# Kernel optimization log

Measured on AMD Instinct MI355X. Metric: run time of the kernel, lower is better.

## Reference

```python
import jax, jax.numpy as jnp
import numpy as np


def _hard_sigmoid(x):
    # torch: clamp(0.2 * x + 0.5, 0, 1)
    return jnp.clip(0.2 * x + 0.5, 0.0, 1.0)


def _hardtanh(x):
    return jnp.clip(x, -1.0, 1.0)


def _run_dir(x, h0, c0, w_ih, w_hh, b):
    """One direction of a HardLSTM layer.
    x: [T, B, I], h0/c0: [B, H], w_ih: [4H, I], w_hh: [4H, H], b: [4H]
    (b is bias_ih + bias_hh of the original cell; identical math).
    """
    # Hoist the input projection out of the recurrence (one big GEMM).
    gx = jnp.einsum('tbi,gi->tbg', x, w_ih) + b  # [T, B, 4H]

    def step(carry, gx_t):
        h, c = carry
        gates = gx_t + h @ w_hh.T  # [B, 4H]
        i, f, g, o = jnp.split(gates, 4, axis=-1)
        i = _hard_sigmoid(i)
        f = _hard_sigmoid(f)
        g = _hardtanh(g)
        o = _hard_sigmoid(o)
        cy = f * c + i * g
        hy = o * _hardtanh(cy)
        return (hy, cy), hy

    (h, c), ys = jax.lax.scan(step, (h0, c0), gx)
    return ys, h, c


def _bidir_layer(x, h0, c0, w_ih, w_hh, b):
    """h0/c0: [2, B, H]; w_ih: [2, 4H, I]; w_hh: [2, 4H, H]; b: [2, 4H]."""
    yf, hf, cf = _run_dir(x, h0[0], c0[0], w_ih[0], w_hh[0], b[0])
    yb, hb, cb = _run_dir(x[::-1], h0[1], c0[1], w_ih[1], w_hh[1], b[1])
    yb = yb[::-1]
    # torch cat([yf.unsqueeze(2), yb.unsqueeze(2)], 2).view(T, B, 2H)
    y = jnp.concatenate([yf, yb], axis=-1)  # [T, B, 2H]
    return y, jnp.stack([hf, hb]), jnp.stack([cf, cb])


def reference(x, h0, c0, w_ih0, w_hh0, b0, w_ih1, w_hh1, b1):
    # Stacked 2-layer bidirectional HardLSTM, time-major input.
    y0, h_l0, c_l0 = _bidir_layer(x, h0[0:2], c0[0:2], w_ih0, w_hh0, b0)
    y1, h_l1, c_l1 = _bidir_layer(y0, h0[2:4], c0[2:4], w_ih1, w_hh1, b1)
    hn = jnp.concatenate([h_l0, h_l1], axis=0)  # [4, B, H]
    cn = jnp.concatenate([c_l0, c_l1], axis=0)
    return y1, hn, cn


def setup_inputs() -> dict:
    key = jax.random.key(0)
    ks = jax.random.split(key, 8)
    T, B, I, H = 512, 32, 512, 1024
    stdv = 1.0 / np.sqrt(H)  # matches reset_parameters uniform(-stdv, stdv) scale
    FGB = 1.0  # forget_gate_bias

    x = jax.random.normal(ks[0], (T, B, I), dtype=jnp.float32)
    h0 = jnp.zeros((4, B, H), dtype=jnp.float32)
    c0 = jnp.zeros((4, B, H), dtype=jnp.float32)

    def mk_w(k, shape):
        return (jax.random.normal(k, shape, dtype=jnp.float32) * stdv).astype(jnp.float32)

    w_ih0 = mk_w(ks[1], (2, 4 * H, I))
    w_hh0 = mk_w(ks[2], (2, 4 * H, H))
    b0 = mk_w(ks[3], (2, 4 * H))
    w_ih1 = mk_w(ks[4], (2, 4 * H, 2 * H))
    w_hh1 = mk_w(ks[5], (2, 4 * H, H))
    b1 = mk_w(ks[6], (2, 4 * H))
    # forget gate bias override (bias_ih forget slice = FGB, bias_hh = 0 -> sum = FGB)
    b0 = b0.at[:, H:2 * H].set(FGB)
    b1 = b1.at[:, H:2 * H].set(FGB)

    return {"x": x, "h0": h0, "c0": c0,
            "w_ih0": w_ih0, "w_hh0": w_hh0, "b0": b0,
            "w_ih1": w_ih1, "w_hh1": w_hh1, "b1": b1}
```

## Files before the change

kernel.cpp:

```cpp
#include <hip/hip_runtime.h>
#include <cstdint>


typedef _Float16 half8 __attribute__((ext_vector_type(8)));
typedef _Float16 half4v __attribute__((ext_vector_type(4)));
typedef float floatx4 __attribute__((ext_vector_type(4)));
typedef int int4v __attribute__((ext_vector_type(4)));

#define T_LEN 512
#define BATCH 32
#define HID 1024
#define NTB 16384
#define UPW 16
#define WPD 64

__device__ __forceinline__ float hsig(float x) {
  return fminf(fmaxf(fmaf(0.2f, x, 0.5f), 0.0f), 1.0f);
}
__device__ __forceinline__ float htanh(float x) {
  return fminf(fmaxf(x, -1.0f), 1.0f);
}

__device__ __forceinline__ int4v load_co16(const void* p) {
  int4v r;
  asm volatile("global_load_dwordx4 %0, %1, off sc0 sc1"
               : "=&v"(r) : "v"(p) : "memory");
  return r;
}
__device__ __forceinline__ void store_co16(void* p, int4v v) {
  asm volatile("global_store_dwordx4 %0, %1, off sc0 sc1"
               :: "v"(p), "v"(v) : "memory");
}
__device__ __forceinline__ void waitcnt0() {
  asm volatile("s_waitcnt vmcnt(0)" ::: "memory");
}
__device__ __forceinline__ void barrier_lgkm() {
  asm volatile("s_waitcnt lgkmcnt(0)" ::: "memory");
  __builtin_amdgcn_sched_barrier(0);
  __builtin_amdgcn_s_barrier();
  __builtin_amdgcn_sched_barrier(0);
}

__device__ __forceinline__ void gll16(const void* g, void* l) {
  __builtin_amdgcn_global_load_lds((const __attribute__((address_space(1))) void*)g,
                                   (__attribute__((address_space(3))) void*)l,
                                   16, 0, 0);
}

__device__ __forceinline__ void gate_xpose(floatx4 v, bool i1, bool i0,
                                           float& gI, float& gF,
                                           float& gG, float& gO) {
  float s0 = i1 ? v[0] : v[2], s1 = i1 ? v[1] : v[3];
  float r0 = __shfl_xor(s0, 32), r1 = __shfl_xor(s1, 32);
  float A0 = i1 ? r0 : v[0], A1 = i1 ? r1 : v[1];
  float A2 = i1 ? v[2] : r0, A3 = i1 ? v[3] : r1;
  s0 = i0 ? A0 : A1; s1 = i0 ? A2 : A3;
  r0 = __shfl_xor(s0, 16); r1 = __shfl_xor(s1, 16);
  gI = i0 ? r0 : A0; gF = i0 ? A1 : r0;
  gG = i0 ? r1 : A2; gO = i0 ? A3 : r1;
}

__global__ __launch_bounds__(256) void cvt_f32_f16(const float* __restrict__ s,
                                                   _Float16* __restrict__ d,
                                                   int n4) {
  int i = blockIdx.x * blockDim.x + threadIdx.x;
  int stride = gridDim.x * blockDim.x;
  for (; i < n4; i += stride) {
    float4 v = ((const float4*)s)[i];
    half4v h = {(_Float16)v.x, (_Float16)v.y, (_Float16)v.z, (_Float16)v.w};
    ((half4v*)d)[i] = h;
  }
}

__global__ __launch_bounds__(256) void gemm_gx(const _Float16* __restrict__ A,
                                               const _Float16* __restrict__ B,
                                               const float* __restrict__ bias,
                                               _Float16* __restrict__ C,
                                               int K) {
  __shared__ __align__(16) _Float16 A_s[128 * 64];
  __shared__ __align__(16) _Float16 B_s[128 * 64];
  const int tid = threadIdx.x;
  const int lane = tid & 63;
  const int w = tid >> 6;
  const int bm = blockIdx.x >> 7;
  const int bn = blockIdx.x & 127;
  const int m0 = bm * 128, n0 = bn * 128;

  floatx4 acc[4][4] = {};

  const int srow = w * 8 + (lane >> 3);
  const int scol = ((lane & 7) ^ ((lane >> 3) & 7)) * 8;
  const _Float16* Ag = A + (size_t)(m0 + srow) * K + scol;
  const _Float16* Bg = B + (size_t)(n0 + srow) * K + scol;
  char* As_base = (char*)A_s + (size_t)(w * 8) * 128;
  char* Bs_base = (char*)B_s + (size_t)(w * 8) * 128;

  const int wm = (w >> 1) * 64;
  const int wn = (w & 1) * 64;
  const int fr = lane & 15;
  const int fk = lane >> 4;

  for (int kb = 0; kb < K; kb += 64) {
#pragma unroll
    for (int i = 0; i < 4; ++i) {
      gll16(Ag + (size_t)i * 32 * K + kb, As_base + i * 32 * 128);
      gll16(Bg + (size_t)i * 32 * K + kb, Bs_base + i * 32 * 128);
    }
    __syncthreads();
#pragma unroll
    for (int kt = 0; kt < 2; ++kt) {
      half8 af[4], bf[4];
#pragma unroll
      for (int mi = 0; mi < 4; ++mi) {
        int row = wm + mi * 16 + fr;
        int k8 = kt * 4 + fk;
        af[mi] = *(const half8*)(A_s + row * 64 + ((k8 ^ (row & 7)) << 3));
      }
#pragma unroll
      for (int ni = 0; ni < 4; ++ni) {
        int row = wn + ni * 16 + fr;
        int k8 = kt * 4 + fk;
        bf[ni] = *(const half8*)(B_s + row * 64 + ((k8 ^ (row & 7)) << 3));
      }
#pragma unroll
      for (int mi = 0; mi < 4; ++mi)
#pragma unroll
        for (int ni = 0; ni < 4; ++ni)
          acc[mi][ni] = __builtin_amdgcn_mfma_f32_16x16x32_f16(af[mi], bf[ni],
                                                               acc[mi][ni], 0, 0, 0);
    }
    __syncthreads();
  }

#pragma unroll
  for (int mi = 0; mi < 4; ++mi) {
    int rowb = m0 + wm + mi * 16 + fk * 4;
#pragma unroll
    for (int r = 0; r < 4; ++r) {
      float bv = bias[rowb + r];
#pragma unroll
      for (int ni = 0; ni < 4; ++ni) {
        int col = n0 + wn + ni * 16 + fr;
        C[(size_t)(rowb + r) * NTB + col] = (_Float16)(acc[mi][ni][r] + bv);
      }
    }
  }
}

__global__ __launch_bounds__(512) void recur(const _Float16* __restrict__ gx,
                                             const _Float16* __restrict__ whh,
                                             const float* __restrict__ h0,
                                             const float* __restrict__ c0,
                                             _Float16* __restrict__ hbuf,
                                             int* __restrict__ flags,
                                             int layer,
                                             _Float16* __restrict__ yf16,
                                             float* __restrict__ yf32,
                                             float* __restrict__ hn,
                                             float* __restrict__ cn) {
  __shared__ __align__(16) _Float16 h_s[BATCH * HID];
  __shared__ __align__(16) _Float16 hout_s[BATCH * UPW];

  const int tid = threadIdx.x;
  const int lane = tid & 63;
  const int w = tid >> 6;
  const int wu = w >> 1, wn = w & 1;
  const int dir = blockIdx.x >> 6;
  const int wgd = blockIdx.x & 63;
  const int u0 = wgd * UPW;
  const int fr = lane & 15, fk = lane >> 4;

  half8 af[32];
  {
    const int g = fr >> 2, du = fr & 3;
    const _Float16* wrow = whh + ((size_t)dir * 4096 + g * 1024 + u0 + wu * 4 + du) * HID;
#pragma unroll
    for (int kt = 0; kt < 32; ++kt)
      af[kt] = *(const half8*)(wrow + kt * 32 + fk * 8);
  }

  const int unit = u0 + wu * 4 + fk;
  const int bat  = wn * 16 + fr;
  const size_t st0 = (size_t)(layer * 2 + dir) * (BATCH * HID);
  float c = c0[st0 + (size_t)bat * HID + unit];

  _Float16* buf0 = hbuf + (size_t)dir * (BATCH * HID);
  _Float16* buf1 = hbuf + (size_t)(2 + dir) * (BATCH * HID);
  int* fl = flags + dir * WPD;

  hout_s[bat * UPW + wu * 4 + fk] = (_Float16)h0[st0 + (size_t)bat * HID + unit];
  __syncthreads();
  if (w == 0) {
    int b = lane >> 1, hf = lane & 1;
    int4v v = *(const int4v*)(hout_s + b * UPW + hf * 8);
    store_co16(buf0 + (size_t)b * HID + u0 + hf * 8, v);
    waitcnt0();
    if (lane == 0) {
      int fv = 1;
      asm volatile("global_store_dword %0, %1, off sc0 sc1"
                   :: "v"(fl + wgd), "v"(fv) : "memory");
    }
  }

  const size_t GS = (size_t)1024 * NTB;
  const _Float16* gxp = gx + ((size_t)dir * 4096 + unit) * NTB;

  int ts0 = dir ? (T_LEN - 1) : 0;
  float gxi = (float)gxp[0 * GS + (size_t)ts0 * BATCH + bat];
  float gxf = (float)gxp[1 * GS + (size_t)ts0 * BATCH + bat];
  float gxg = (float)gxp[2 * GS + (size_t)ts0 * BATCH + bat];
  float gxo = (float)gxp[3 * GS + (size_t)ts0 * BATCH + bat];

  const bool i1 = (fk >> 1) & 1, i0 = fk & 1;

  for (int t = 0; t < T_LEN; ++t) {
    if (w == 0) {
      const int want = t + 1;
      for (;;) {
        int v;
        asm volatile("global_load_dword %0, %1, off sc0 sc1\n\ts_waitcnt vmcnt(0)"
                     : "=&v"(v) : "v"(fl + lane) : "memory");
        if (__all(v >= want)) break;
        __builtin_amdgcn_s_sleep(1);
      }
    }
    barrier_lgkm();

    const _Float16* src = (t & 1) ? buf1 : buf0;
    _Float16* dst = (t & 1) ? buf0 : buf1;

    int4v hv[8];
#pragma unroll
    for (int i = 0; i < 8; ++i)
      hv[i] = load_co16((const char*)src + (size_t)(i * 512 + tid) * 16);
    waitcnt0();
#pragma unroll
    for (int i = 0; i < 8; ++i) {
      int cbyte = (i * 512 + tid) * 16;
      int b = cbyte >> 11;
      int slot = cbyte & 2047;
      *(int4v*)((char*)h_s + b * 2048 + (slot ^ ((b & 7) << 4))) = hv[i];
    }

    int tn = (t + 1 < T_LEN) ? t + 1 : t;
    int tsn = dir ? (T_LEN - 1 - tn) : tn;
    float ngxi = (float)gxp[0 * GS + (size_t)tsn * BATCH + bat];
    float ngxf = (float)gxp[1 * GS + (size_t)tsn * BATCH + bat];
    float ngxg = (float)gxp[2 * GS + (size_t)tsn * BATCH + bat];
    float ngxo = (float)gxp[3 * GS + (size_t)tsn * BATCH + bat];

    barrier_lgkm();

    floatx4 acc0 = {0.f, 0.f, 0.f, 0.f}, acc1 = {0.f, 0.f, 0.f, 0.f};
    {
      const char* hp = (const char*)h_s + bat * 2048;
      const int bx = (bat & 7) << 4;
#pragma unroll
      for (int kt = 0; kt < 32; kt += 2) {
        half8 b0 = *(const half8*)(hp + ((kt * 64 + fk * 16) ^ bx));
        half8 b1 = *(const half8*)(hp + (((kt + 1) * 64 + fk * 16) ^ bx));
        acc0 = __builtin_amdgcn_mfma_f32_16x16x32_f16(af[kt], b0, acc0, 0, 0, 0);
        acc1 = __builtin_amdgcn_mfma_f32_16x16x32_f16(af[kt + 1], b1, acc1, 0, 0, 0);
      }
    }
    floatx4 v = acc0 + acc1;

    float gI, gF, gG, gO;
    gate_xpose(v, i1, i0, gI, gF, gG, gO);

    float ig = hsig(gI + gxi);
    float fg = hsig(gF + gxf);
    float gg = htanh(gG + gxg);
    float og = hsig(gO + gxo);
    c = fg * c + ig * gg;
    float h = og * htanh(c);

    hout_s[bat * UPW + wu * 4 + fk] = (_Float16)h;

    const int tseq = dir ? (T_LEN - 1 - t) : t;
    size_t yidx = ((size_t)tseq * BATCH + bat) * 2048 + (size_t)dir * 1024 + unit;
    if (yf16) yf16[yidx] = (_Float16)h;
    else      yf32[yidx] = h;

    gxi = ngxi; gxf = ngxf; gxg = ngxg; gxo = ngxo;

    if (t == T_LEN - 1) {
      size_t o = st0 + (size_t)bat * HID + unit;
      hn[o] = h;
      cn[o] = c;
    } else {
      barrier_lgkm();
      if (w == 0) {
        int b = lane >> 1, hf = lane & 1;
        int4v vv = *(const int4v*)(hout_s + b * UPW + hf * 8);
        store_co16(dst + (size_t)b * HID + u0 + hf * 8, vv);
        waitcnt0();
        if (lane == 0) {
          int fv = t + 2;
          asm volatile("global_store_dword %0, %1, off sc0 sc1"
                       :: "v"(fl + wgd), "v"(fv) : "memory");
        }
      }
    }
  }
}

extern "C" void kernel_launch(void* const* d_in, const int* in_sizes, int n_in,
                              void* d_out, int out_size, void* d_ws, size_t ws_size,
                              hipStream_t stream) {
  const float* x    = (const float*)d_in[0];
  const float* h0   = (const float*)d_in[1];
  const float* c0   = (const float*)d_in[2];
  const float* wih0 = (const float*)d_in[3];
  const float* whh0 = (const float*)d_in[4];
  const float* b0   = (const float*)d_in[5];
  const float* wih1 = (const float*)d_in[6];
  const float* whh1 = (const float*)d_in[7];
  const float* b1   = (const float*)d_in[8];
  float* out = (float*)d_out;

  char* ws = (char*)d_ws;
  size_t off = 0;
  int* flags = (int*)ws;                      off += 4096;
  _Float16* xh    = (_Float16*)(ws + off);    off += (size_t)8388608 * 2;
  _Float16* wih0h = (_Float16*)(ws + off);    off += (size_t)4194304 * 2;
  _Float16* whh0h = (_Float16*)(ws + off);    off += (size_t)8388608 * 2;
  _Float16* wih1h = (_Float16*)(ws + off);    off += (size_t)16777216 * 2;
  _Float16* whh1h = (_Float16*)(ws + off);    off += (size_t)8388608 * 2;
  _Float16* y0h   = (_Float16*)(ws + off);    off += (size_t)33554432 * 2;
  _Float16* hbuf  = (_Float16*)(ws + off);    off += (size_t)131072 * 2;
  _Float16* gxbuf = (_Float16*)(ws + off);    off += (size_t)134217728 * 2;

  hipMemsetAsync(flags, 0, 4096, stream);

  cvt_f32_f16<<<2048, 256, 0, stream>>>(x,    xh,    8388608 / 4);
  cvt_f32_f16<<<2048, 256, 0, stream>>>(wih0, wih0h, 4194304 / 4);
  cvt_f32_f16<<<2048, 256, 0, stream>>>(whh0, whh0h, 8388608 / 4);
  cvt_f32_f16<<<2048, 256, 0, stream>>>(wih1, wih1h, 16777216 / 4);
  cvt_f32_f16<<<2048, 256, 0, stream>>>(whh1, whh1h, 8388608 / 4);

  float* hn = out + 33554432;
  float* cn = out + 33685504;

  gemm_gx<<<8192, 256, 0, stream>>>(wih0h, xh, b0, gxbuf, 512);
  recur<<<128, 512, 0, stream>>>(gxbuf, whh0h, h0, c0, hbuf, flags, 0,
                                 y0h, nullptr, hn, cn);
  gemm_gx<<<8192, 256, 0, stream>>>(wih1h, y0h, b1, gxbuf, 2048);
  recur<<<128, 512, 0, stream>>>(gxbuf, whh1h, h0, c0, hbuf, flags + 128, 1,
                                 nullptr, out, hn, cn);
}
```

Before: 6.393 ms.

## Replace flag-based grid sync with tagged self-validating h chunks

Drops the separate flag array and the wave-0 spin-then-load handshake. Each wave now publishes its h values in 16-byte chunks that carry the step tag in the first and last dwords, so consumers poll the data itself and scatter it into LDS once both tags match. This removes a round trip (flag poll, then data load) and the LDS staging and barrier on the producer side. In exchange, every thread spin-loads its 256 bytes repeatedly, which adds polling traffic, and correctness depends on each 16-byte store being seen atomically.

```diff
diff --git a/kernel.cpp b/kernel.cpp
--- a/kernel.cpp
+++ b/kernel.cpp
@@ -6,6 +6,7 @@
 typedef _Float16 half4v __attribute__((ext_vector_type(4)));
 typedef float floatx4 __attribute__((ext_vector_type(4)));
 typedef int int4v __attribute__((ext_vector_type(4)));
+typedef int int2v __attribute__((ext_vector_type(2)));
 
 #define T_LEN 512
 #define BATCH 32
@@ -13,6 +14,7 @@
 #define NTB 16384
 #define UPW 16
 #define WPD 64
+#define CHUNKS_DIR 8192
 
 __device__ __forceinline__ float hsig(float x) {
   return fminf(fmaxf(fmaf(0.2f, x, 0.5f), 0.0f), 1.0f);
@@ -58,6 +60,20 @@
   r0 = __shfl_xor(s0, 16); r1 = __shfl_xor(s1, 16);
   gI = i0 ? r0 : A0; gF = i0 ? A1 : r0;
   gG = i0 ? r1 : A2; gO = i0 ? A3 : r1;
+}
+
+__device__ __forceinline__ void publish_h(float h, int tag, char* cb,
+                                          int wgd, int w, int fr, int fk) {
+  union { _Float16 f; unsigned short u; } cv; cv.f = (_Float16)h;
+  int hb = (int)cv.u;
+  int p = __shfl_xor(hb, 16);
+  int d01 = (fk & 1) ? ((p & 0xffff) | (hb << 16))
+                     : ((hb & 0xffff) | (p << 16));
+  int d23 = __shfl_xor(d01, 32);
+  if (fk == 0) {
+    int4v v = {tag, d01, d23, tag};
+    store_co16(cb + (size_t)(wgd * 128 + w * 16 + fr) * 16, v);
+  }
 }
 
 __global__ __launch_bounds__(256) void cvt_f32_f16(const float* __restrict__ s,
@@ -151,15 +167,13 @@
                                              const _Float16* __restrict__ whh,
                                              const float* __restrict__ h0,
                                              const float* __restrict__ c0,
-                                             _Float16* __restrict__ hbuf,
-                                             int* __restrict__ flags,
+                                             char* __restrict__ chunkbuf,
                                              int layer,
                                              _Float16* __restrict__ yf16,
                                              float* __restrict__ yf32,
                                              float* __restrict__ hn,
                                              float* __restrict__ cn) {
   __shared__ __align__(16) _Float16 h_s[BATCH * HID];
-  __shared__ __align__(16) _Float16 hout_s[BATCH * UPW];
 
   const int tid = threadIdx.x;
   const int lane = tid & 63;
@@ -170,6 +184,9 @@
   const int u0 = wgd * UPW;
   const int fr = lane & 15, fk = lane >> 4;
 
+  char* cb0 = chunkbuf + (size_t)(dir * 2 + 0) * CHUNKS_DIR * 16;
+  char* cb1 = chunkbuf + (size_t)(dir * 2 + 1) * CHUNKS_DIR * 16;
+
   half8 af[32];
   {
     const int g = fr >> 2, du = fr & 3;
@@ -184,23 +201,7 @@
   const size_t st0 = (size_t)(layer * 2 + dir) * (BATCH * HID);
   float c = c0[st0 + (size_t)bat * HID + unit];
 
-  _Float16* buf0 = hbuf + (size_t)dir * (BATCH * HID);
-  _Float16* buf1 = hbuf + (size_t)(2 + dir) * (BATCH * HID);
-  int* fl = flags + dir * WPD;
-
-  hout_s[bat * UPW + wu * 4 + fk] = (_Float16)h0[st0 + (size_t)bat * HID + unit];
-  __syncthreads();
-  if (w == 0) {
-    int b = lane >> 1, hf = lane & 1;
-    int4v v = *(const int4v*)(hout_s + b * UPW + hf * 8);
-    store_co16(buf0 + (size_t)b * HID + u0 + hf * 8, v);
-    waitcnt0();
-    if (lane == 0) {
-      int fv = 1;
-      asm volatile("global_store_dword %0, %1, off sc0 sc1"
-                   :: "v"(fl + wgd), "v"(fv) : "memory");
-    }
-  }
+  publish_h(h0[st0 + (size_t)bat * HID + unit], 1, cb0, wgd, w, fr, fk);
 
   const size_t GS = (size_t)1024 * NTB;
   const _Float16* gxp = gx + ((size_t)dir * 4096 + unit) * NTB;
@@ -214,32 +215,30 @@
   const bool i1 = (fk >> 1) & 1, i0 = fk & 1;
 
   for (int t = 0; t < T_LEN; ++t) {
-    if (w == 0) {
-      const int want = t + 1;
-      for (;;) {
-        int v;
-        asm volatile("global_load_dword %0, %1, off sc0 sc1\n\ts_waitcnt vmcnt(0)"
-                     : "=&v"(v) : "v"(fl + lane) : "memory");
-        if (__all(v >= want)) break;
-        __builtin_amdgcn_s_sleep(1);
-      }
-    }
-    barrier_lgkm();
-
-    const _Float16* src = (t & 1) ? buf1 : buf0;
-    _Float16* dst = (t & 1) ? buf0 : buf1;
-
-    int4v hv[8];
-#pragma unroll
-    for (int i = 0; i < 8; ++i)
-      hv[i] = load_co16((const char*)src + (size_t)(i * 512 + tid) * 16);
-    waitcnt0();
-#pragma unroll
-    for (int i = 0; i < 8; ++i) {
-      int cbyte = (i * 512 + tid) * 16;
-      int b = cbyte >> 11;
-      int slot = cbyte & 2047;
-      *(int4v*)((char*)h_s + b * 2048 + (slot ^ ((b & 7) << 4))) = hv[i];
+    const int want = t + 1;
+    const char* src = ((t & 1) ? cb1 : cb0) + (size_t)tid * 256;
+
+    int4v val[16];
+    for (;;) {
+#pragma unroll
+      for (int i = 0; i < 16; ++i) val[i] = load_co16(src + i * 16);
+      waitcnt0();
+      bool ok = true;
+#pragma unroll
+      for (int i = 0; i < 16; ++i)
+        ok &= (val[i][0] == want) & (val[i][3] == want);
+      if (ok) break;
+      __builtin_amdgcn_s_sleep(2);
+    }
+#pragma unroll
+    for (int i = 0; i < 16; ++i) {
+      int G = tid * 16 + i;
+      int wg2 = G >> 7, cc = G & 127;
+      int bat2 = ((cc >> 4) & 1) * 16 + (cc & 15);
+      int uh = cc >> 5;
+      int slot = wg2 * 2 + (uh >> 1);
+      int lds_b = bat2 * 2048 + ((slot * 16) ^ ((bat2 & 7) << 4)) + (uh & 1) * 8;
+      *(int2v*)((char*)h_s + lds_b) = (int2v){val[i][1], val[i][2]};
     }
 
     int tn = (t + 1 < T_LEN) ? t + 1 : t;
@@ -275,8 +274,6 @@
     c = fg * c + ig * gg;
     float h = og * htanh(c);
 
-    hout_s[bat * UPW + wu * 4 + fk] = (_Float16)h;
-
     const int tseq = dir ? (T_LEN - 1 - t) : t;
     size_t yidx = ((size_t)tseq * BATCH + bat) * 2048 + (size_t)dir * 1024 + unit;
     if (yf16) yf16[yidx] = (_Float16)h;
@@ -289,19 +286,10 @@
       hn[o] = h;
       cn[o] = c;
     } else {
-      barrier_lgkm();
-      if (w == 0) {
-        int b = lane >> 1, hf = lane & 1;
-        int4v vv = *(const int4v*)(hout_s + b * UPW + hf * 8);
-        store_co16(dst + (size_t)b * HID + u0 + hf * 8, vv);
-        waitcnt0();
-        if (lane == 0) {
-          int fv = t + 2;
-          asm volatile("global_store_dword %0, %1, off sc0 sc1"
-                       :: "v"(fl + wgd), "v"(fv) : "memory");
-        }
-      }
-    }
+      publish_h(h, t + 2, ((t + 1) & 1) ? cb1 : cb0, wgd, w, fr, fk);
+    }
+
+    barrier_lgkm();
   }
 }
 
@@ -321,17 +309,16 @@
 
   char* ws = (char*)d_ws;
   size_t off = 0;
-  int* flags = (int*)ws;                      off += 4096;
+  char* chunkbuf = ws;                        off += (size_t)2 * 2 * 2 * CHUNKS_DIR * 16;
   _Float16* xh    = (_Float16*)(ws + off);    off += (size_t)8388608 * 2;
   _Float16* wih0h = (_Float16*)(ws + off);    off += (size_t)4194304 * 2;
   _Float16* whh0h = (_Float16*)(ws + off);    off += (size_t)8388608 * 2;
   _Float16* wih1h = (_Float16*)(ws + off);    off += (size_t)16777216 * 2;
   _Float16* whh1h = (_Float16*)(ws + off);    off += (size_t)8388608 * 2;
   _Float16* y0h   = (_Float16*)(ws + off);    off += (size_t)33554432 * 2;
-  _Float16* hbuf  = (_Float16*)(ws + off);    off += (size_t)131072 * 2;
   _Float16* gxbuf = (_Float16*)(ws + off);    off += (size_t)134217728 * 2;
 
-  hipMemsetAsync(flags, 0, 4096, stream);
+  hipMemsetAsync(chunkbuf, 0, (size_t)2 * 2 * 2 * CHUNKS_DIR * 16, stream);
 
   cvt_f32_f16<<<2048, 256, 0, stream>>>(x,    xh,    8388608 / 4);
   cvt_f32_f16<<<2048, 256, 0, stream>>>(wih0, wih0h, 4194304 / 4);
@@ -342,10 +329,13 @@
   float* hn = out + 33554432;
   float* cn = out + 33685504;
 
+  char* cb_l0 = chunkbuf;
+  char* cb_l1 = chunkbuf + (size_t)2 * 2 * CHUNKS_DIR * 16;
+
   gemm_gx<<<8192, 256, 0, stream>>>(wih0h, xh, b0, gxbuf, 512);
-  recur<<<128, 512, 0, stream>>>(gxbuf, whh0h, h0, c0, hbuf, flags, 0,
+  recur<<<128, 512, 0, stream>>>(gxbuf, whh0h, h0, c0, cb_l0, 0,
                                  y0h, nullptr, hn, cn);
   gemm_gx<<<8192, 256, 0, stream>>>(wih1h, y0h, b1, gxbuf, 2048);
-  recur<<<128, 512, 0, stream>>>(gxbuf, whh1h, h0, c0, hbuf, flags + 128, 1,
+  recur<<<128, 512, 0, stream>>>(gxbuf, whh1h, h0, c0, cb_l1, 1,
                                  nullptr, out, hn, cn);
 }
```

After: 15.90 ms. 149% more time.

## Exchange recurrent hidden state as uint8 with fp16 magic-number decode

Applied to the files above, without the earlier changes.

The hidden state passed between workgroups through global memory is quantized to 8 bits (h*127+128), halving the per-step global exchange traffic. On load, bytes are expanded into fp16 values of the form 1024+q using a byte-permute with 0x64 high bytes. W_hh is prescaled by 1/127, and the accumulator is initialized with a per-row bias correction (1152 times the row sum) to cancel the offset. This trades hidden-state precision (about 8 bits) for lower latency in the serial recurrence, and also adds a launch-bounds occupancy hint and moves the buffer to the front of the workspace.

```diff
diff --git a/kernel.cpp b/kernel.cpp
--- a/kernel.cpp
+++ b/kernel.cpp
@@ -6,6 +6,7 @@
 typedef _Float16 half4v __attribute__((ext_vector_type(4)));
 typedef float floatx4 __attribute__((ext_vector_type(4)));
 typedef int int4v __attribute__((ext_vector_type(4)));
+typedef int int2v __attribute__((ext_vector_type(2)));
 
 #define T_LEN 512
 #define BATCH 32
@@ -27,8 +28,8 @@
                : "=&v"(r) : "v"(p) : "memory");
   return r;
 }
-__device__ __forceinline__ void store_co16(void* p, int4v v) {
-  asm volatile("global_store_dwordx4 %0, %1, off sc0 sc1"
+__device__ __forceinline__ void store_co8(void* p, int2v v) {
+  asm volatile("global_store_dwordx2 %0, %1, off sc0 sc1"
                :: "v"(p), "v"(v) : "memory");
 }
 __device__ __forceinline__ void waitcnt0() {
@@ -147,19 +148,19 @@
   }
 }
 
-__global__ __launch_bounds__(512) void recur(const _Float16* __restrict__ gx,
-                                             const _Float16* __restrict__ whh,
-                                             const float* __restrict__ h0,
-                                             const float* __restrict__ c0,
-                                             _Float16* __restrict__ hbuf,
-                                             int* __restrict__ flags,
-                                             int layer,
-                                             _Float16* __restrict__ yf16,
-                                             float* __restrict__ yf32,
-                                             float* __restrict__ hn,
-                                             float* __restrict__ cn) {
+__global__ __launch_bounds__(512, 2) void recur(const _Float16* __restrict__ gx,
+                                                const _Float16* __restrict__ whh,
+                                                const float* __restrict__ h0,
+                                                const float* __restrict__ c0,
+                                                unsigned char* __restrict__ hbuf,
+                                                int* __restrict__ flags,
+                                                int layer,
+                                                _Float16* __restrict__ yf16,
+                                                float* __restrict__ yf32,
+                                                float* __restrict__ hn,
+                                                float* __restrict__ cn) {
   __shared__ __align__(16) _Float16 h_s[BATCH * HID];
-  __shared__ __align__(16) _Float16 hout_s[BATCH * UPW];
+  __shared__ __align__(16) unsigned char hout_s[BATCH * UPW];
 
   const int tid = threadIdx.x;
   const int lane = tid & 63;
@@ -171,29 +172,49 @@
   const int fr = lane & 15, fk = lane >> 4;
 
   half8 af[32];
+  float rowsum = 0.f;
   {
     const int g = fr >> 2, du = fr & 3;
     const _Float16* wrow = whh + ((size_t)dir * 4096 + g * 1024 + u0 + wu * 4 + du) * HID;
 #pragma unroll
-    for (int kt = 0; kt < 32; ++kt)
-      af[kt] = *(const half8*)(wrow + kt * 32 + fk * 8);
-  }
+    for (int kt = 0; kt < 32; ++kt) {
+      half8 raw = *(const half8*)(wrow + kt * 32 + fk * 8);
+      half8 s;
+#pragma unroll
+      for (int e = 0; e < 8; ++e) {
+        float v = (float)raw[e] * (1.f / 127.f);
+        s[e] = (_Float16)v;
+        rowsum += (float)s[e];
+      }
+      af[kt] = s;
+    }
+  }
+  rowsum += __shfl_xor(rowsum, 16);
+  rowsum += __shfl_xor(rowsum, 32);
+  float corr0 = 1152.f * __shfl(rowsum, fk * 4 + 0);
+  float corr1 = 1152.f * __shfl(rowsum, fk * 4 + 1);
+  float corr2 = 1152.f * __shfl(rowsum, fk * 4 + 2);
+  float corr3 = 1152.f * __shfl(rowsum, fk * 4 + 3);
 
   const int unit = u0 + wu * 4 + fk;
   const int bat  = wn * 16 + fr;
   const size_t st0 = (size_t)(layer * 2 + dir) * (BATCH * HID);
   float c = c0[st0 + (size_t)bat * HID + unit];
 
-  _Float16* buf0 = hbuf + (size_t)dir * (BATCH * HID);
-  _Float16* buf1 = hbuf + (size_t)(2 + dir) * (BATCH * HID);
+  unsigned char* buf0 = hbuf + (size_t)dir * 32768;
+  unsigned char* buf1 = hbuf + (size_t)(2 + dir) * 32768;
   int* fl = flags + dir * WPD;
 
-  hout_s[bat * UPW + wu * 4 + fk] = (_Float16)h0[st0 + (size_t)bat * HID + unit];
+  {
+    float hv0 = h0[st0 + (size_t)bat * HID + unit];
+    int q = (int)rintf(fminf(fmaxf(hv0, -1.f), 1.f) * 127.f) + 128;
+    hout_s[bat * UPW + wu * 4 + fk] = (unsigned char)q;
+  }
   __syncthreads();
   if (w == 0) {
     int b = lane >> 1, hf = lane & 1;
-    int4v v = *(const int4v*)(hout_s + b * UPW + hf * 8);
-    store_co16(buf0 + (size_t)b * HID + u0 + hf * 8, v);
+    int2v v2 = *(const int2v*)(hout_s + lane * 8);
+    store_co8(buf0 + (size_t)b * HID + u0 + hf * 8, v2);
     waitcnt0();
     if (lane == 0) {
       int fv = 1;
@@ -212,6 +233,7 @@
   float gxo = (float)gxp[3 * GS + (size_t)ts0 * BATCH + bat];
 
   const bool i1 = (fk >> 1) & 1, i0 = fk & 1;
+  const unsigned c64 = 0x64646464u;
 
   for (int t = 0; t < T_LEN; ++t) {
     if (w == 0) {
@@ -226,20 +248,31 @@
     }
     barrier_lgkm();
 
-    const _Float16* src = (t & 1) ? buf1 : buf0;
-    _Float16* dst = (t & 1) ? buf0 : buf1;
-
-    int4v hv[8];
-#pragma unroll
-    for (int i = 0; i < 8; ++i)
-      hv[i] = load_co16((const char*)src + (size_t)(i * 512 + tid) * 16);
+    const unsigned char* src = (t & 1) ? buf1 : buf0;
+    unsigned char* dst = (t & 1) ? buf0 : buf1;
+
+    int4v u8v[4];
+#pragma unroll
+    for (int cc = 0; cc < 4; ++cc)
+      u8v[cc] = load_co16(src + cc * 8192 + tid * 16);
     waitcnt0();
 #pragma unroll
-    for (int i = 0; i < 8; ++i) {
-      int cbyte = (i * 512 + tid) * 16;
-      int b = cbyte >> 11;
-      int slot = cbyte & 2047;
-      *(int4v*)((char*)h_s + b * 2048 + (slot ^ ((b & 7) << 4))) = hv[i];
+    for (int cc = 0; cc < 4; ++cc) {
+      int b = cc * 8 + w;
+      int lslot = lane * 2;
+      char* row = (char*)h_s + b * 2048;
+      int swz = (b & 7) << 4;
+      int4v A, B2;
+      A[0]  = __builtin_amdgcn_perm(c64, (unsigned)u8v[cc][0], 0x05010400u);
+      A[1]  = __builtin_amdgcn_perm(c64, (unsigned)u8v[cc][0], 0x07030602u);
+      A[2]  = __builtin_amdgcn_perm(c64, (unsigned)u8v[cc][1], 0x05010400u);
+      A[3]  = __builtin_amdgcn_perm(c64, (unsigned)u8v[cc][1], 0x07030602u);
+      B2[0] = __builtin_amdgcn_perm(c64, (unsigned)u8v[cc][2], 0x05010400u);
+      B2[1] = __builtin_amdgcn_perm(c64, (unsigned)u8v[cc][2], 0x07030602u);
+      B2[2] = __builtin_amdgcn_perm(c64, (unsigned)u8v[cc][3], 0x05010400u);
+      B2[3] = __builtin_amdgcn_perm(c64, (unsigned)u8v[cc][3], 0x07030602u);
+      *(int4v*)(row + ((lslot * 16) ^ swz)) = A;
+      *(int4v*)(row + (((lslot + 1) * 16) ^ swz)) = B2;
     }
 
     int tn = (t + 1 < T_LEN) ? t + 1 : t;
@@ -251,7 +284,8 @@
 
     barrier_lgkm();
 
-    floatx4 acc0 = {0.f, 0.f, 0.f, 0.f}, acc1 = {0.f, 0.f, 0.f, 0.f};
+    floatx4 acc0 = {-corr0, -corr1, -corr2, -corr3};
+    floatx4 acc1 = {0.f, 0.f, 0.f, 0.f};
     {
       const char* hp = (const char*)h_s + bat * 2048;
       const int bx = (bat & 7) << 4;
@@ -275,7 +309,10 @@
     c = fg * c + ig * gg;
     float h = og * htanh(c);
 
-    hout_s[bat * UPW + wu * 4 + fk] = (_Float16)h;
+    {
+      int q = (int)rintf(h * 127.f) + 128;
+      hout_s[bat * UPW + wu * 4 + fk] = (unsigned char)q;
+    }
 
     const int tseq = dir ? (T_LEN - 1 - t) : t;
     size_t yidx = ((size_t)tseq * BATCH + bat) * 2048 + (size_t)dir * 1024 + unit;
@@ -292,8 +329,8 @@
       barrier_lgkm();
       if (w == 0) {
         int b = lane >> 1, hf = lane & 1;
-        int4v vv = *(const int4v*)(hout_s + b * UPW + hf * 8);
-        store_co16(dst + (size_t)b * HID + u0 + hf * 8, vv);
+        int2v v2 = *(const int2v*)(hout_s + lane * 8);
+        store_co8(dst + (size_t)b * HID + u0 + hf * 8, v2);
         waitcnt0();
         if (lane == 0) {
           int fv = t + 2;
@@ -321,14 +358,14 @@
 
   char* ws = (char*)d_ws;
   size_t off = 0;
-  int* flags = (int*)ws;                      off += 4096;
+  int* flags = (int*)ws;                          off += 4096;
+  unsigned char* hbuf = (unsigned char*)(ws + off); off += 262144;
   _Float16* xh    = (_Float16*)(ws + off);    off += (size_t)8388608 * 2;
   _Float16* wih0h = (_Float16*)(ws + off);    off += (size_t)4194304 * 2;
   _Float16* whh0h = (_Float16*)(ws + off);    off += (size_t)8388608 * 2;
   _Float16* wih1h = (_Float16*)(ws + off);    off += (size_t)16777216 * 2;
   _Float16* whh1h = (_Float16*)(ws + off);    off += (size_t)8388608 * 2;
   _Float16* y0h   = (_Float16*)(ws + off);    off += (size_t)33554432 * 2;
-  _Float16* hbuf  = (_Float16*)(ws + off);    off += (size_t)131072 * 2;
   _Float16* gxbuf = (_Float16*)(ws + off);    off += (size_t)134217728 * 2;
 
   hipMemsetAsync(flags, 0, 4096, stream);
@@ -346,6 +383,6 @@
   recur<<<128, 512, 0, stream>>>(gxbuf, whh0h, h0, c0, hbuf, flags, 0,
                                  y0h, nullptr, hn, cn);
   gemm_gx<<<8192, 256, 0, stream>>>(wih1h, y0h, b1, gxbuf, 2048);
-  recur<<<128, 512, 0, stream>>>(gxbuf, whh1h, h0, c0, hbuf, flags + 128, 1,
+  recur<<<128, 512, 0, stream>>>(gxbuf, whh1h, h0, c0, hbuf + 131072, flags + 128, 1,
                                  nullptr, out, hn, cn);
 }
```

Measured after the change: 6.016 ms. 1.06x faster.
